# Kernel optimization log

Measured on AMD Instinct MI355X. Metric: run time of the kernel, lower is better.

The kernel has to match this reference:

```python
import jax, jax.numpy as jnp
import numpy as np

# nuScenes-scale config: batch 2, 360x360 BEV grid (1440/4), 128 channels,
# 10 classes, 200 proposals, 3x3 NMS kernel, 40k occupied voxels per sample.
B, H, W_GRID, NUM_CLS, NUM_PROP, NMS_K = 2, 360, 360, 10, 200, 3
C = 128
N_PER_B = 40000
NEG_FILL = -1000000.0  # scatter_nd fill value from to_dense()


def _bev_pos():
    # replicates create_2D_grid: coord = (x_index_along_dim1, y_index_along_dim0)
    xs = jnp.arange(H, dtype=jnp.float32)
    ys = jnp.arange(W_GRID, dtype=jnp.float32)
    by, bx = jnp.meshgrid(xs, ys, indexing='ij')  # by[i,j]=i, bx[i,j]=j
    return jnp.stack([bx, by], axis=-1).reshape(-1, 2)  # [H*W, 2]


def setup_inputs() -> dict:
    key = jax.random.key(0)
    ks = jax.random.split(key, 10)
    # unique spatial locations per batch sample (sparse voxel coords)
    flats = [jax.random.permutation(ks[i], H * W_GRID)[:N_PER_B] for i in range(B)]
    flat = jnp.concatenate(flats)
    b = jnp.repeat(jnp.arange(B), N_PER_B)
    indices = jnp.stack([b, flat // W_GRID, flat % W_GRID], axis=1).astype(jnp.int32)
    features = jax.random.normal(ks[4], (B * N_PER_B, C), jnp.float32)
    # heatmap head (pointwise linears standing in for the submconv stack)
    W_hm1 = jax.random.normal(ks[5], (C, C), jnp.float32) * (2.0 / C) ** 0.5
    b_hm1 = jnp.zeros((C,), jnp.float32)
    W_hm2 = jax.random.normal(ks[6], (C, NUM_CLS), jnp.float32) * (2.0 / C) ** 0.5
    b_hm2 = jnp.full((NUM_CLS,), -2.19, jnp.float32)  # fc[-1].bias.fill_(-2.19)
    # class_encoding: nn.Conv1d(num_class, channels, 1)
    W_cls = jax.random.normal(ks[7], (C, NUM_CLS), jnp.float32) * 0.1
    b_cls = jnp.zeros((C,), jnp.float32)
    return dict(features=features, W_hm1=W_hm1, b_hm1=b_hm1, W_hm2=W_hm2,
                b_hm2=b_hm2, W_cls=W_cls, b_cls=b_cls, indices=indices)


def reference(features, W_hm1, b_hm1, W_hm2, b_hm2, W_cls, b_cls, indices):
    bidx, yi, xi = indices[:, 0], indices[:, 1], indices[:, 2]
    HW = H * W_GRID

    # --- x.dense(): scatter voxel features to dense BEV grid (zero fill) ---
    xd = jnp.zeros((B, H, W_GRID, C), features.dtype).at[bidx, yi, xi].set(features)
    x_flat = xd.reshape(B, HW, C).transpose(0, 2, 1)  # [B, C, HW]

    # --- heatmap head (per-voxel) then to_dense() with -1e6 fill ---
    hm = jax.nn.relu(features @ W_hm1 + b_hm1) @ W_hm2 + b_hm2  # [N, NUM_CLS]
    dense_hm = jnp.full((B, H, W_GRID, NUM_CLS), NEG_FILL, hm.dtype)
    dense_hm = dense_hm.at[bidx, yi, xi].set(hm).transpose(0, 3, 1, 2)  # [B,K,H,W]

    heat = jax.nn.sigmoid(dense_hm)  # detached in original

    # --- NMS-kernel peak extraction ---
    pad = NMS_K // 2
    inner = jax.lax.reduce_window(heat, -jnp.inf, jax.lax.max,
                                  (1, 1, NMS_K, NMS_K), (1, 1, 1, 1), 'VALID')
    local_max = jnp.zeros_like(heat).at[:, :, pad:H - pad, pad:W_GRID - pad].set(inner)
    # pedestrian (8) and traffic_cone (9): kernel size 1
    local_max = local_max.at[:, 8].set(heat[:, 8]).at[:, 9].set(heat[:, 9])
    heat = heat * (heat == local_max)
    heat_f = heat.reshape(B, NUM_CLS, HW)

    # --- top-k proposals over (class, location) ---
    _, top = jax.lax.top_k(heat_f.reshape(B, -1), NUM_PROP)  # [B, P]
    cls = top // HW
    idx = top % HW

    # --- gather proposal features + class encoding ---
    qf = jnp.take_along_axis(x_flat, jnp.broadcast_to(idx[:, None, :], (B, C, NUM_PROP)), axis=2)
    onehot = jax.nn.one_hot(cls, NUM_CLS, dtype=qf.dtype)  # [B, P, K]
    qf = qf + jnp.einsum('ck,bpk->bcp', W_cls, onehot) + b_cls[None, :, None]

    # --- proposal positions and heatmap scores ---
    query_pos = _bev_pos()[idx]  # [B, P, 2]
    qhs = jnp.take_along_axis(heat_f, jnp.broadcast_to(idx[:, None, :], (B, NUM_CLS, NUM_PROP)), axis=2)
    return qf, query_pos, qhs, cls
```

## Files before the change

kernel.cpp:

```cpp
#include <hip/hip_runtime.h>

#define HW 129600
#define WG 360
#define HG 360
#define NCLS 10
#define NPROP 200
#define CDIM 128
#define NROWS 80000
#define NB 2
#define NPB (NROWS / NB)
#define SEL_CAP 4096
#define HBINS 4096
#define RPB 64
#define PSTR 12
#define BPB 32

__device__ __align__(16) const float ZROW[12] = {0.f, 0.f, 0.f, 0.f, 0.f, 0.f,
                                                 0.f, 0.f, 0.f, 0.f, 0.f, 0.f};

__device__ __forceinline__ void lds_cp16(float* l, const float* g) {
  __builtin_amdgcn_global_load_lds(
      (const __attribute__((address_space(1))) void*)g,
      (__attribute__((address_space(3))) void*)l, 16, 0, 0);
}

__device__ __forceinline__ float4 fmax4(float4 a, float4 b) {
  float4 r;
  r.x = fmaxf(a.x, b.x);
  r.y = fmaxf(a.y, b.y);
  r.z = fmaxf(a.z, b.z);
  r.w = fmaxf(a.w, b.w);
  return r;
}

__global__ __launch_bounds__(256, 4) void k_head(
    const float* __restrict__ feat, const float* __restrict__ W1,
    const float* __restrict__ b1, const float* __restrict__ W2,
    const float* __restrict__ b2, const int* __restrict__ idxs,
    float* __restrict__ val_raw, int* __restrict__ rowmap,
    unsigned int* __restrict__ hist, int* __restrict__ sel_cnt) {
  __shared__ __align__(16) float lds_w[3][16 * 128];
  __shared__ __align__(16) float lds_f[3][RPB * 16];
  const int tid = threadIdx.x;
  const int row0 = blockIdx.x * RPB;
  const int tc = tid & 31;
  const int tr = tid >> 5;
  const int wv = tid >> 6;
  const int lane = tid & 63;

  auto stage = [&](int kt, int nb) {
#pragma unroll
    for (int c = 0; c < 2; ++c) {
      const int off = (wv * 2 + c) * 256;
      lds_cp16(&lds_w[nb][off], W1 + kt * 2048 + off + lane * 4);
    }
    {
      const int off = wv * 256;
      const int fidx = off + lane * 4;
      const int r = fidx >> 4, kk = fidx & 15;
      lds_cp16(&lds_f[nb][off],
               feat + (size_t)(row0 + r) * CDIM + kt * 16 + kk);
    }
  };

  stage(0, 0);
  stage(1, 1);
  if (blockIdx.x == 0) {
    uint4* h4 = (uint4*)hist;
    for (int i = tid; i < (NB * HBINS) / 4; i += 256)
      h4[i] = make_uint4(0u, 0u, 0u, 0u);
    if (tid < 2) sel_cnt[tid] = 0;
  }
  if (tid < RPB) {
    int row = row0 + tid;
    int bb = idxs[row * 3 + 0];
    int yy = idxs[row * 3 + 1];
    int xx = idxs[row * 3 + 2];
    rowmap[(size_t)bb * HW + yy * WG + xx] = row;
  }

  float acc[8][4];
#pragma unroll
  for (int r = 0; r < 8; ++r)
#pragma unroll
    for (int c = 0; c < 4; ++c) acc[r][c] = 0.f;

#pragma unroll
  for (int kt = 0; kt < 8; ++kt) {
    const int cb = kt % 3;
    if (kt < 7) {
      asm volatile("s_waitcnt vmcnt(3)" ::: "memory");
    } else {
      asm volatile("s_waitcnt vmcnt(0)" ::: "memory");
    }
    __builtin_amdgcn_sched_barrier(0);
    __builtin_amdgcn_s_barrier();
    __builtin_amdgcn_sched_barrier(0);
    if (kt < 6) stage(kt + 2, (kt + 2) % 3);
#pragma unroll
    for (int kg = 0; kg < 4; ++kg) {
      float4 w0 = *(const float4*)(&lds_w[cb][(kg * 4 + 0) * 128 + tc * 4]);
      float4 w1 = *(const float4*)(&lds_w[cb][(kg * 4 + 1) * 128 + tc * 4]);
      float4 w2 = *(const float4*)(&lds_w[cb][(kg * 4 + 2) * 128 + tc * 4]);
      float4 w3 = *(const float4*)(&lds_w[cb][(kg * 4 + 3) * 128 + tc * 4]);
#pragma unroll
      for (int r = 0; r < 8; ++r) {
        float4 fv = *(const float4*)(&lds_f[cb][(tr * 8 + r) * 16 + kg * 4]);
        acc[r][0] = fmaf(fv.x, w0.x, acc[r][0]);
        acc[r][0] = fmaf(fv.y, w1.x, acc[r][0]);
        acc[r][0] = fmaf(fv.z, w2.x, acc[r][0]);
        acc[r][0] = fmaf(fv.w, w3.x, acc[r][0]);
        acc[r][1] = fmaf(fv.x, w0.y, acc[r][1]);
        acc[r][1] = fmaf(fv.y, w1.y, acc[r][1]);
        acc[r][1] = fmaf(fv.z, w2.y, acc[r][1]);
        acc[r][1] = fmaf(fv.w, w3.y, acc[r][1]);
        acc[r][2] = fmaf(fv.x, w0.z, acc[r][2]);
        acc[r][2] = fmaf(fv.y, w1.z, acc[r][2]);
        acc[r][2] = fmaf(fv.z, w2.z, acc[r][2]);
        acc[r][2] = fmaf(fv.w, w3.z, acc[r][2]);
        acc[r][3] = fmaf(fv.x, w0.w, acc[r][3]);
        acc[r][3] = fmaf(fv.y, w1.w, acc[r][3]);
        acc[r][3] = fmaf(fv.z, w2.w, acc[r][3]);
        acc[r][3] = fmaf(fv.w, w3.w, acc[r][3]);
      }
    }
  }
  __syncthreads();

  float* w2t = &lds_f[0][0];
  for (int i = tid; i < CDIM * NCLS; i += 256) {
    int k = i / NCLS, j = i - k * NCLS;
    w2t[j * 128 + k] = W2[i];
  }
  __syncthreads();

  float* hbuf = &lds_w[0][0];
  float4 b1v = *(const float4*)(b1 + tc * 4);
#pragma unroll
  for (int half = 0; half < 2; ++half) {
    if ((tr >> 2) == half) {
      int ltr = tr & 3;
#pragma unroll
      for (int r = 0; r < 8; ++r) {
        float4 h;
        h.x = fmaxf(acc[r][0] + b1v.x, 0.f);
        h.y = fmaxf(acc[r][1] + b1v.y, 0.f);
        h.z = fmaxf(acc[r][2] + b1v.z, 0.f);
        h.w = fmaxf(acc[r][3] + b1v.w, 0.f);
        *(float4*)(hbuf + (ltr * 8 + r) * 128 + tc * 4) = h;
      }
    }
    __syncthreads();
    for (int o = tid; o < 32 * NCLS; o += 256) {
      int r = o / NCLS, j = o - r * NCLS;
      float s = b2[j];
      for (int i4 = 0; i4 < 32; ++i4) {
        int k4 = (i4 + tid) & 31;
        float4 hv = *(const float4*)(hbuf + r * 128 + k4 * 4);
        float4 wv2 = *(const float4*)(w2t + j * 128 + k4 * 4);
        s = fmaf(hv.x, wv2.x, s);
        s = fmaf(hv.y, wv2.y, s);
        s = fmaf(hv.z, wv2.z, s);
        s = fmaf(hv.w, wv2.w, s);
      }
      float heat = 1.0f / (1.0f + expf(-s));
      int gr = half * 32 + r;
      val_raw[(size_t)(row0 + gr) * PSTR + j] = heat;
    }
    __syncthreads();
  }
}

__global__ __launch_bounds__(256) void k_hist(
    const float* __restrict__ val_raw, const int* __restrict__ idxs,
    const int* __restrict__ rowmap, float* __restrict__ val,
    unsigned int* __restrict__ hist) {
  __shared__ unsigned int lh[HBINS];
  const int tid = threadIdx.x;
  const int row = blockIdx.x * 256 + tid;
  const int blk_b = (blockIdx.x * 256 >= NPB) ? 1 : 0;
  for (int i = tid; i < HBINS; i += 256) lh[i] = 0;
  __syncthreads();

  float v[10];
  int bb = 0;
  const bool valid = row < NROWS;
  if (valid) {
    bb = (row >= NPB) ? 1 : 0;
    const int y = idxs[row * 3 + 1];
    const int x = idxs[row * 3 + 2];
    const int pos = y * WG + x;
    const float* cbase = val_raw + (size_t)row * PSTR;
    float4 c0 = *(const float4*)(cbase + 0);
    float4 c1 = *(const float4*)(cbase + 4);
    float2 c89 = *(const float2*)(cbase + 8);
    const bool interior = (y > 0 && y < HG - 1 && x > 0 && x < WG - 1);
    if (interior) {
      const int dyA[8] = {0, 0, -1, -1, -1, 1, 1, 1};
      const int dxA[8] = {-1, 1, -1, 0, 1, -1, 0, 1};
      float4 m0 = c0, m1 = c1;
      const int* rmb = rowmap + (size_t)bb * HW + pos;
#pragma unroll
      for (int n = 0; n < 8; ++n) {
        const int nrow = rmb[dyA[n] * WG + dxA[n]];
        bool ok =
            ((unsigned)nrow < NROWS) && ((nrow >= NPB) == (bb == 1));
        if (ok) {
          ok = (idxs[nrow * 3 + 1] == y + dyA[n]) &&
               (idxs[nrow * 3 + 2] == x + dxA[n]);
        }
        const float* p = ok ? (val_raw + (size_t)nrow * PSTR) : ZROW;
        m0 = fmax4(m0, *(const float4*)(p + 0));
        m1 = fmax4(m1, *(const float4*)(p + 4));
      }
      v[0] = (c0.x == m0.x) ? c0.x : 0.f;
      v[1] = (c0.y == m0.y) ? c0.y : 0.f;
      v[2] = (c0.z == m0.z) ? c0.z : 0.f;
      v[3] = (c0.w == m0.w) ? c0.w : 0.f;
      v[4] = (c1.x == m1.x) ? c1.x : 0.f;
      v[5] = (c1.y == m1.y) ? c1.y : 0.f;
      v[6] = (c1.z == m1.z) ? c1.z : 0.f;
      v[7] = (c1.w == m1.w) ? c1.w : 0.f;
    } else {
      v[0] = v[1] = v[2] = v[3] = v[4] = v[5] = v[6] = v[7] = 0.f;
    }
    v[8] = c89.x;
    v[9] = c89.y;
    float4 s0 = {v[0], v[1], v[2], v[3]};
    float4 s1 = {v[4], v[5], v[6], v[7]};
    float4 s2 = {v[8], v[9], 0.f, 0.f};
    *(float4*)(val + (size_t)row * PSTR + 0) = s0;
    *(float4*)(val + (size_t)row * PSTR + 4) = s1;
    *(float4*)(val + (size_t)row * PSTR + 8) = s2;
#pragma unroll
    for (int c = 0; c < 10; ++c) {
      if (v[c] > 0.f) {
        unsigned int bin = __float_as_uint(v[c]) >> 18;
        if (bb == blk_b)
          atomicAdd(&lh[bin], 1u);
        else
          atomicAdd(&hist[(size_t)bb * HBINS + bin], 1u);
      }
    }
  }
  __syncthreads();
  unsigned int* gh = hist + (size_t)blk_b * HBINS;
  for (int i = tid; i < HBINS; i += 256) {
    unsigned int c = lh[i];
    if (c) atomicAdd(&gh[i], c);
  }
}

__global__ __launch_bounds__(256) void k_collect(
    const float* __restrict__ val, const int* __restrict__ idxs,
    const unsigned int* __restrict__ hist, unsigned long long* __restrict__ sel,
    int* __restrict__ sel_cnt) {
  __shared__ unsigned int coarse[256];
  __shared__ unsigned int fine16[16];
  __shared__ int sT[2];
  __shared__ int sCi[2];
  const int tid = threadIdx.x;
  for (int bb = 0; bb < NB; ++bb) {
    const unsigned int* h = hist + (size_t)bb * HBINS;
    const uint4* h4 = (const uint4*)(h + tid * 16);
    unsigned int s = 0;
#pragma unroll
    for (int i = 0; i < 4; ++i) {
      uint4 q = h4[i];
      s += q.x + q.y + q.z + q.w;
    }
    if (tid == 0) {
      sCi[bb] = -1;
      sT[bb] = 0;
    }
    coarse[tid] = s;
    __syncthreads();
#pragma unroll
    for (int off = 1; off < 256; off <<= 1) {
      unsigned int vv = (tid + off < 256) ? coarse[tid + off] : 0u;
      __syncthreads();
      coarse[tid] += vv;
      __syncthreads();
    }
    if (coarse[tid] >= NPROP) atomicMax(&sCi[bb], tid);
    __syncthreads();
    const int ci = sCi[bb];
    if (ci >= 0) {
      if (tid < 16) fine16[tid] = h[ci * 16 + tid];
      __syncthreads();
      if (tid == 0) {
        unsigned int cum = (ci + 1 < 256) ? coarse[ci + 1] : 0u;
        int t = 15;
        for (; t > 0; --t) {
          unsigned int c = fine16[t];
          if (cum + c >= NPROP) break;
          cum += c;
        }
        sT[bb] = ci * 16 + t;
      }
    }
    __syncthreads();
  }
  const int row = blockIdx.x * 256 + tid;
  const bool valid = row < NROWS;
  const int bb = (valid && row >= NPB) ? 1 : 0;
  const int T = sT[bb];
  float v[12];
  int pos = 0;
  if (valid) {
    *(float4*)(v + 0) = *(const float4*)(val + (size_t)row * PSTR + 0);
    *(float4*)(v + 4) = *(const float4*)(val + (size_t)row * PSTR + 4);
    *(float4*)(v + 8) = *(const float4*)(val + (size_t)row * PSTR + 8);
    pos = idxs[row * 3 + 1] * WG + idxs[row * 3 + 2];
  }
  const int lane = tid & 63;
#pragma unroll
  for (int cl = 0; cl < 10; ++cl) {
    float vv = valid ? v[cl] : 0.f;
    unsigned int bits = __float_as_uint(vv);
    bool pred = (vv > 0.f) && ((int)(bits >> 18) >= T);
    unsigned long long m0 = __ballot(pred && (bb == 0));
    unsigned long long m1 = __ballot(pred && (bb == 1));
    if (pred) {
      unsigned long long mask = bb ? m1 : m0;
      int leader = __ffsll((unsigned long long)mask) - 1;
      int lb = __popcll(mask & ((1ull << lane) - 1ull));
      int base = 0;
      if (lane == leader) base = atomicAdd(&sel_cnt[bb], (int)__popcll(mask));
      base = __shfl(base, leader, 64);
      unsigned int gidx = (unsigned int)cl * HW + (unsigned int)pos;
      unsigned long long key =
          ((unsigned long long)bits << 32) | (unsigned long long)(~gidx);
      int slot = base + lb;
      if (slot < SEL_CAP) sel[(size_t)bb * SEL_CAP + slot] = key;
    }
  }
}

__global__ __launch_bounds__(256) void k_final(
    const unsigned long long* __restrict__ sel, const int* __restrict__ sel_cnt,
    const float* __restrict__ val, const int* __restrict__ rowmap,
    const float* __restrict__ feat, const float* __restrict__ Wc,
    const float* __restrict__ bc, float* __restrict__ out) {
  __shared__ unsigned long long sk[SEL_CAP];
  __shared__ unsigned long long winners[NPROP];
  __shared__ int wcls[NPROP];
  __shared__ int wrow[NPROP];
  const int b = blockIdx.x / BPB;
  const int part = blockIdx.x % BPB;
  const int tid = threadIdx.x;
  int M = sel_cnt[b];
  if (M > SEL_CAP) M = SEL_CAP;
  for (int i = tid; i < M; i += 256) sk[i] = sel[(size_t)b * SEL_CAP + i];
  __syncthreads();
  for (int i = tid; i < M; i += 256) {
    unsigned long long key = sk[i];
    int rank = 0;
    for (int j = 0; j < M; ++j) rank += (sk[j] > key) ? 1 : 0;
    if (rank < NPROP) winners[rank] = key;
  }
  __syncthreads();
  if (tid < NPROP) {
    unsigned long long key = winners[tid];
    unsigned int gidx = ~((unsigned int)(key & 0xFFFFFFFFull));
    int cls = (int)(gidx / HW);
    int pos = (int)(gidx - (unsigned int)cls * HW);
    wcls[tid] = cls;
    wrow[tid] = rowmap[(size_t)b * HW + pos];
    if (part == 0) {
      int y = pos / WG, x = pos - y * WG;
      out[51200 + ((size_t)b * NPROP + tid) * 2 + 0] = (float)x;
      out[51200 + ((size_t)b * NPROP + tid) * 2 + 1] = (float)y;
      out[56000 + b * NPROP + tid] = (float)cls;
    }
  }
  __syncthreads();
  for (int o = part * 256 + tid; o < NCLS * NPROP; o += BPB * 256) {
    int j = o / NPROP, pp = o - j * NPROP;
    out[52000 + (size_t)b * NCLS * NPROP + o] = val[(size_t)wrow[pp] * PSTR + j];
  }
  for (int o = part * 256 + tid; o < CDIM * NPROP; o += BPB * 256) {
    int c = o / NPROP, pp = o - c * NPROP;
    out[(size_t)b * CDIM * NPROP + o] =
        feat[(size_t)wrow[pp] * CDIM + c] + Wc[c * NCLS + wcls[pp]] + bc[c];
  }
}

extern "C" void kernel_launch(void* const* d_in, const int* in_sizes, int n_in,
                              void* d_out, int out_size, void* d_ws,
                              size_t ws_size, hipStream_t stream) {
  const float* feat = (const float*)d_in[0];
  const float* W1 = (const float*)d_in[1];
  const float* b1 = (const float*)d_in[2];
  const float* W2 = (const float*)d_in[3];
  const float* b2 = (const float*)d_in[4];
  const float* Wc = (const float*)d_in[5];
  const float* bc = (const float*)d_in[6];
  const int* idxs = (const int*)d_in[7];
  float* out = (float*)d_out;

  char* ws = (char*)d_ws;
  unsigned int* hist = (unsigned int*)(ws + 0);
  int* rowmap = (int*)(ws + 32768);
  unsigned long long* sel = (unsigned long long*)(ws + 1069568);
  int* sel_cnt = (int*)(ws + 1135104);
  float* val_raw = (float*)(ws + 1135120);
  float* val = (float*)(ws + 4975120);

  k_head<<<NROWS / RPB, 256, 0, stream>>>(feat, W1, b1, W2, b2, idxs, val_raw,
                                          rowmap, hist, sel_cnt);
  k_hist<<<(NROWS + 255) / 256, 256, 0, stream>>>(val_raw, idxs, rowmap, val,
                                                  hist);
  k_collect<<<(NROWS + 255) / 256, 256, 0, stream>>>(val, idxs, hist, sel,
                                                     sel_cnt);
  k_final<<<NB * BPB, 256, 0, stream>>>(sel, sel_cnt, val, rowmap, feat, Wc, bc,
                                        out);
}
```

Measured before the change: 173.5 us.

## Fuse candidate collection into final top-k kernel with per-block LDS selection

Merges the candidate-collection and final ranking kernels into one. Each final block now computes the histogram threshold for its batch, scans all rows of that batch itself, and appends candidates to shared memory with LDS atomics. This removes one kernel launch, the global selection buffer and its counter, and the global atomics. The cost is that each of the 32 blocks per batch redundantly scans the whole batch. That is a long serial loop per block with little memory parallelism.

```diff
diff --git a/kernel.cpp b/kernel.cpp
--- a/kernel.cpp
+++ b/kernel.cpp
@@ -38,7 +38,7 @@
     const float* __restrict__ b1, const float* __restrict__ W2,
     const float* __restrict__ b2, const int* __restrict__ idxs,
     float* __restrict__ val_raw, int* __restrict__ rowmap,
-    unsigned int* __restrict__ hist, int* __restrict__ sel_cnt) {
+    unsigned int* __restrict__ hist) {
   __shared__ __align__(16) float lds_w[3][16 * 128];
   __shared__ __align__(16) float lds_f[3][RPB * 16];
   const int tid = threadIdx.x;
@@ -69,7 +69,6 @@
     uint4* h4 = (uint4*)hist;
     for (int i = tid; i < (NB * HBINS) / 4; i += 256)
       h4[i] = make_uint4(0u, 0u, 0u, 0u);
-    if (tid < 2) sel_cnt[tid] = 0;
   }
   if (tid < RPB) {
     int row = row0 + tid;
@@ -171,7 +170,7 @@
   }
 }
 
-__global__ __launch_bounds__(256) void k_hist(
+__global__ __launch_bounds__(256) void k_nms(
     const float* __restrict__ val_raw, const int* __restrict__ idxs,
     const int* __restrict__ rowmap, float* __restrict__ val,
     unsigned int* __restrict__ hist) {
@@ -251,17 +250,29 @@
   }
 }
 
-__global__ __launch_bounds__(256) void k_collect(
+__global__ __launch_bounds__(256) void k_sel(
     const float* __restrict__ val, const int* __restrict__ idxs,
-    const unsigned int* __restrict__ hist, unsigned long long* __restrict__ sel,
-    int* __restrict__ sel_cnt) {
+    const unsigned int* __restrict__ hist, const int* __restrict__ rowmap,
+    const float* __restrict__ feat, const float* __restrict__ Wc,
+    const float* __restrict__ bc, float* __restrict__ out) {
+  __shared__ unsigned long long sk[SEL_CAP];
+  __shared__ unsigned long long winners[NPROP];
+  __shared__ int wcls[NPROP];
+  __shared__ int wrow[NPROP];
   __shared__ unsigned int coarse[256];
   __shared__ unsigned int fine16[16];
-  __shared__ int sT[2];
-  __shared__ int sCi[2];
+  __shared__ int sT1, sCi1, lcnt;
+  const int b = blockIdx.x / BPB;
+  const int part = blockIdx.x % BPB;
   const int tid = threadIdx.x;
-  for (int bb = 0; bb < NB; ++bb) {
-    const unsigned int* h = hist + (size_t)bb * HBINS;
+
+  if (tid == 0) {
+    sCi1 = -1;
+    sT1 = 0;
+    lcnt = 0;
+  }
+  {
+    const unsigned int* h = hist + (size_t)b * HBINS;
     const uint4* h4 = (const uint4*)(h + tid * 16);
     unsigned int s = 0;
 #pragma unroll
@@ -269,24 +280,22 @@
       uint4 q = h4[i];
       s += q.x + q.y + q.z + q.w;
     }
-    if (tid == 0) {
-      sCi[bb] = -1;
-      sT[bb] = 0;
-    }
     coarse[tid] = s;
-    __syncthreads();
-#pragma unroll
-    for (int off = 1; off < 256; off <<= 1) {
-      unsigned int vv = (tid + off < 256) ? coarse[tid + off] : 0u;
-      __syncthreads();
-      coarse[tid] += vv;
-      __syncthreads();
-    }
-    if (coarse[tid] >= NPROP) atomicMax(&sCi[bb], tid);
-    __syncthreads();
-    const int ci = sCi[bb];
+  }
+  __syncthreads();
+#pragma unroll
+  for (int off = 1; off < 256; off <<= 1) {
+    unsigned int vv = (tid + off < 256) ? coarse[tid + off] : 0u;
+    __syncthreads();
+    coarse[tid] += vv;
+    __syncthreads();
+  }
+  if (coarse[tid] >= NPROP) atomicMax(&sCi1, tid);
+  __syncthreads();
+  {
+    const int ci = sCi1;
     if (ci >= 0) {
-      if (tid < 16) fine16[tid] = h[ci * 16 + tid];
+      if (tid < 16) fine16[tid] = hist[(size_t)b * HBINS + ci * 16 + tid];
       __syncthreads();
       if (tid == 0) {
         unsigned int cum = (ci + 1 < 256) ? coarse[ci + 1] : 0u;
@@ -296,63 +305,38 @@
           if (cum + c >= NPROP) break;
           cum += c;
         }
-        sT[bb] = ci * 16 + t;
-      }
-    }
-    __syncthreads();
-  }
-  const int row = blockIdx.x * 256 + tid;
-  const bool valid = row < NROWS;
-  const int bb = (valid && row >= NPB) ? 1 : 0;
-  const int T = sT[bb];
-  float v[12];
-  int pos = 0;
-  if (valid) {
-    *(float4*)(v + 0) = *(const float4*)(val + (size_t)row * PSTR + 0);
-    *(float4*)(v + 4) = *(const float4*)(val + (size_t)row * PSTR + 4);
-    *(float4*)(v + 8) = *(const float4*)(val + (size_t)row * PSTR + 8);
-    pos = idxs[row * 3 + 1] * WG + idxs[row * 3 + 2];
-  }
-  const int lane = tid & 63;
-#pragma unroll
-  for (int cl = 0; cl < 10; ++cl) {
-    float vv = valid ? v[cl] : 0.f;
-    unsigned int bits = __float_as_uint(vv);
-    bool pred = (vv > 0.f) && ((int)(bits >> 18) >= T);
-    unsigned long long m0 = __ballot(pred && (bb == 0));
-    unsigned long long m1 = __ballot(pred && (bb == 1));
-    if (pred) {
-      unsigned long long mask = bb ? m1 : m0;
-      int leader = __ffsll((unsigned long long)mask) - 1;
-      int lb = __popcll(mask & ((1ull << lane) - 1ull));
-      int base = 0;
-      if (lane == leader) base = atomicAdd(&sel_cnt[bb], (int)__popcll(mask));
-      base = __shfl(base, leader, 64);
-      unsigned int gidx = (unsigned int)cl * HW + (unsigned int)pos;
-      unsigned long long key =
-          ((unsigned long long)bits << 32) | (unsigned long long)(~gidx);
-      int slot = base + lb;
-      if (slot < SEL_CAP) sel[(size_t)bb * SEL_CAP + slot] = key;
-    }
-  }
-}
-
-__global__ __launch_bounds__(256) void k_final(
-    const unsigned long long* __restrict__ sel, const int* __restrict__ sel_cnt,
-    const float* __restrict__ val, const int* __restrict__ rowmap,
-    const float* __restrict__ feat, const float* __restrict__ Wc,
-    const float* __restrict__ bc, float* __restrict__ out) {
-  __shared__ unsigned long long sk[SEL_CAP];
-  __shared__ unsigned long long winners[NPROP];
-  __shared__ int wcls[NPROP];
-  __shared__ int wrow[NPROP];
-  const int b = blockIdx.x / BPB;
-  const int part = blockIdx.x % BPB;
-  const int tid = threadIdx.x;
-  int M = sel_cnt[b];
+        sT1 = ci * 16 + t;
+      }
+    }
+    __syncthreads();
+  }
+  const int T = sT1;
+
+  for (int r = tid; r < NPB; r += 256) {
+    const int row = b * NPB + r;
+    float4 a0 = *(const float4*)(val + (size_t)row * PSTR + 0);
+    float4 a1 = *(const float4*)(val + (size_t)row * PSTR + 4);
+    float2 a2 = *(const float2*)(val + (size_t)row * PSTR + 8);
+    const float v[10] = {a0.x, a0.y, a0.z, a0.w, a1.x,
+                         a1.y, a1.z, a1.w, a2.x, a2.y};
+    const int pos = idxs[row * 3 + 1] * WG + idxs[row * 3 + 2];
+#pragma unroll
+    for (int cl = 0; cl < 10; ++cl) {
+      unsigned int bits = __float_as_uint(v[cl]);
+      if (v[cl] > 0.f && (int)(bits >> 18) >= T) {
+        int ls = atomicAdd(&lcnt, 1);
+        if (ls < SEL_CAP) {
+          unsigned int gidx = (unsigned int)cl * HW + (unsigned int)pos;
+          sk[ls] =
+              ((unsigned long long)bits << 32) | (unsigned long long)(~gidx);
+        }
+      }
+    }
+  }
+  __syncthreads();
+  int M = lcnt;
   if (M > SEL_CAP) M = SEL_CAP;
-  for (int i = tid; i < M; i += 256) sk[i] = sel[(size_t)b * SEL_CAP + i];
-  __syncthreads();
+
   for (int i = tid; i < M; i += 256) {
     unsigned long long key = sk[i];
     int rank = 0;
@@ -402,17 +386,13 @@
   char* ws = (char*)d_ws;
   unsigned int* hist = (unsigned int*)(ws + 0);
   int* rowmap = (int*)(ws + 32768);
-  unsigned long long* sel = (unsigned long long*)(ws + 1069568);
-  int* sel_cnt = (int*)(ws + 1135104);
-  float* val_raw = (float*)(ws + 1135120);
-  float* val = (float*)(ws + 4975120);
+  float* val_raw = (float*)(ws + 1069568);
+  float* val = (float*)(ws + 4909568);
 
   k_head<<<NROWS / RPB, 256, 0, stream>>>(feat, W1, b1, W2, b2, idxs, val_raw,
-                                          rowmap, hist, sel_cnt);
-  k_hist<<<(NROWS + 255) / 256, 256, 0, stream>>>(val_raw, idxs, rowmap, val,
-                                                  hist);
-  k_collect<<<(NROWS + 255) / 256, 256, 0, stream>>>(val, idxs, hist, sel,
-                                                     sel_cnt);
-  k_final<<<NB * BPB, 256, 0, stream>>>(sel, sel_cnt, val, rowmap, feat, Wc, bc,
-                                        out);
-}
+                                          rowmap, hist);
+  k_nms<<<(NROWS + 255) / 256, 256, 0, stream>>>(val_raw, idxs, rowmap, val,
+                                                 hist);
+  k_sel<<<NB * BPB, 256, 0, stream>>>(val, idxs, hist, rowmap, feat, Wc, bc,
+                                      out);
+}
```

New measurement: 263.0 us. +51.6%, slower.

## Enlarge head GEMM tile to 128 rows with 8x8 per-thread register blocking

Applied to the files above, without the earlier changes.

The first-layer GEMM tile in k_head doubles from 64 to 128 rows per block, and each thread now computes an 8x8 output micro-tile instead of 8x4. The staging, wait counts and the second-layer epilogue (now four quarters) are adjusted to match. This raises arithmetic intensity per LDS load and halves the block count, which cuts the per-block overhead of W1 staging. In exchange it uses more registers and LDS, lowers occupancy (launch bounds drop from 4 to 3) and leaves fewer blocks to spread across CUs.

```diff
diff --git a/kernel.cpp b/kernel.cpp
--- a/kernel.cpp
+++ b/kernel.cpp
@@ -11,7 +11,7 @@
 #define NPB (NROWS / NB)
 #define SEL_CAP 4096
 #define HBINS 4096
-#define RPB 64
+#define RPB 128
 #define PSTR 12
 #define BPB 32
 
@@ -33,7 +33,7 @@
   return r;
 }
 
-__global__ __launch_bounds__(256, 4) void k_head(
+__global__ __launch_bounds__(256, 3) void k_head(
     const float* __restrict__ feat, const float* __restrict__ W1,
     const float* __restrict__ b1, const float* __restrict__ W2,
     const float* __restrict__ b2, const int* __restrict__ idxs,
@@ -43,8 +43,8 @@
   __shared__ __align__(16) float lds_f[3][RPB * 16];
   const int tid = threadIdx.x;
   const int row0 = blockIdx.x * RPB;
-  const int tc = tid & 31;
-  const int tr = tid >> 5;
+  const int tc = tid & 15;
+  const int tr = tid >> 4;
   const int wv = tid >> 6;
   const int lane = tid & 63;
 
@@ -54,8 +54,9 @@
       const int off = (wv * 2 + c) * 256;
       lds_cp16(&lds_w[nb][off], W1 + kt * 2048 + off + lane * 4);
     }
-    {
-      const int off = wv * 256;
+#pragma unroll
+    for (int c = 0; c < 2; ++c) {
+      const int off = (wv * 2 + c) * 256;
       const int fidx = off + lane * 4;
       const int r = fidx >> 4, kk = fidx & 15;
       lds_cp16(&lds_f[nb][off],
@@ -79,17 +80,17 @@
     rowmap[(size_t)bb * HW + yy * WG + xx] = row;
   }
 
-  float acc[8][4];
+  float acc[8][8];
 #pragma unroll
   for (int r = 0; r < 8; ++r)
 #pragma unroll
-    for (int c = 0; c < 4; ++c) acc[r][c] = 0.f;
+    for (int c = 0; c < 8; ++c) acc[r][c] = 0.f;
 
 #pragma unroll
   for (int kt = 0; kt < 8; ++kt) {
     const int cb = kt % 3;
     if (kt < 7) {
-      asm volatile("s_waitcnt vmcnt(3)" ::: "memory");
+      asm volatile("s_waitcnt vmcnt(4)" ::: "memory");
     } else {
       asm volatile("s_waitcnt vmcnt(0)" ::: "memory");
     }
@@ -99,29 +100,49 @@
     if (kt < 6) stage(kt + 2, (kt + 2) % 3);
 #pragma unroll
     for (int kg = 0; kg < 4; ++kg) {
-      float4 w0 = *(const float4*)(&lds_w[cb][(kg * 4 + 0) * 128 + tc * 4]);
-      float4 w1 = *(const float4*)(&lds_w[cb][(kg * 4 + 1) * 128 + tc * 4]);
-      float4 w2 = *(const float4*)(&lds_w[cb][(kg * 4 + 2) * 128 + tc * 4]);
-      float4 w3 = *(const float4*)(&lds_w[cb][(kg * 4 + 3) * 128 + tc * 4]);
+      float4 a0 = *(const float4*)(&lds_w[cb][(kg * 4 + 0) * 128 + tc * 8]);
+      float4 a1 = *(const float4*)(&lds_w[cb][(kg * 4 + 1) * 128 + tc * 8]);
+      float4 a2 = *(const float4*)(&lds_w[cb][(kg * 4 + 2) * 128 + tc * 8]);
+      float4 a3 = *(const float4*)(&lds_w[cb][(kg * 4 + 3) * 128 + tc * 8]);
+      float4 b0 = *(const float4*)(&lds_w[cb][(kg * 4 + 0) * 128 + tc * 8 + 4]);
+      float4 b1q = *(const float4*)(&lds_w[cb][(kg * 4 + 1) * 128 + tc * 8 + 4]);
+      float4 b2q = *(const float4*)(&lds_w[cb][(kg * 4 + 2) * 128 + tc * 8 + 4]);
+      float4 b3q = *(const float4*)(&lds_w[cb][(kg * 4 + 3) * 128 + tc * 8 + 4]);
 #pragma unroll
       for (int r = 0; r < 8; ++r) {
         float4 fv = *(const float4*)(&lds_f[cb][(tr * 8 + r) * 16 + kg * 4]);
-        acc[r][0] = fmaf(fv.x, w0.x, acc[r][0]);
-        acc[r][0] = fmaf(fv.y, w1.x, acc[r][0]);
-        acc[r][0] = fmaf(fv.z, w2.x, acc[r][0]);
-        acc[r][0] = fmaf(fv.w, w3.x, acc[r][0]);
-        acc[r][1] = fmaf(fv.x, w0.y, acc[r][1]);
-        acc[r][1] = fmaf(fv.y, w1.y, acc[r][1]);
-        acc[r][1] = fmaf(fv.z, w2.y, acc[r][1]);
-        acc[r][1] = fmaf(fv.w, w3.y, acc[r][1]);
-        acc[r][2] = fmaf(fv.x, w0.z, acc[r][2]);
-        acc[r][2] = fmaf(fv.y, w1.z, acc[r][2]);
-        acc[r][2] = fmaf(fv.z, w2.z, acc[r][2]);
-        acc[r][2] = fmaf(fv.w, w3.z, acc[r][2]);
-        acc[r][3] = fmaf(fv.x, w0.w, acc[r][3]);
-        acc[r][3] = fmaf(fv.y, w1.w, acc[r][3]);
-        acc[r][3] = fmaf(fv.z, w2.w, acc[r][3]);
-        acc[r][3] = fmaf(fv.w, w3.w, acc[r][3]);
+        acc[r][0] = fmaf(fv.x, a0.x, acc[r][0]);
+        acc[r][0] = fmaf(fv.y, a1.x, acc[r][0]);
+        acc[r][0] = fmaf(fv.z, a2.x, acc[r][0]);
+        acc[r][0] = fmaf(fv.w, a3.x, acc[r][0]);
+        acc[r][1] = fmaf(fv.x, a0.y, acc[r][1]);
+        acc[r][1] = fmaf(fv.y, a1.y, acc[r][1]);
+        acc[r][1] = fmaf(fv.z, a2.y, acc[r][1]);
+        acc[r][1] = fmaf(fv.w, a3.y, acc[r][1]);
+        acc[r][2] = fmaf(fv.x, a0.z, acc[r][2]);
+        acc[r][2] = fmaf(fv.y, a1.z, acc[r][2]);
+        acc[r][2] = fmaf(fv.z, a2.z, acc[r][2]);
+        acc[r][2] = fmaf(fv.w, a3.z, acc[r][2]);
+        acc[r][3] = fmaf(fv.x, a0.w, acc[r][3]);
+        acc[r][3] = fmaf(fv.y, a1.w, acc[r][3]);
+        acc[r][3] = fmaf(fv.z, a2.w, acc[r][3]);
+        acc[r][3] = fmaf(fv.w, a3.w, acc[r][3]);
+        acc[r][4] = fmaf(fv.x, b0.x, acc[r][4]);
+        acc[r][4] = fmaf(fv.y, b1q.x, acc[r][4]);
+        acc[r][4] = fmaf(fv.z, b2q.x, acc[r][4]);
+        acc[r][4] = fmaf(fv.w, b3q.x, acc[r][4]);
+        acc[r][5] = fmaf(fv.x, b0.y, acc[r][5]);
+        acc[r][5] = fmaf(fv.y, b1q.y, acc[r][5]);
+        acc[r][5] = fmaf(fv.z, b2q.y, acc[r][5]);
+        acc[r][5] = fmaf(fv.w, b3q.y, acc[r][5]);
+        acc[r][6] = fmaf(fv.x, b0.z, acc[r][6]);
+        acc[r][6] = fmaf(fv.y, b1q.z, acc[r][6]);
+        acc[r][6] = fmaf(fv.z, b2q.z, acc[r][6]);
+        acc[r][6] = fmaf(fv.w, b3q.z, acc[r][6]);
+        acc[r][7] = fmaf(fv.x, b0.w, acc[r][7]);
+        acc[r][7] = fmaf(fv.y, b1q.w, acc[r][7]);
+        acc[r][7] = fmaf(fv.z, b2q.w, acc[r][7]);
+        acc[r][7] = fmaf(fv.w, b3q.w, acc[r][7]);
       }
     }
   }
@@ -135,19 +156,26 @@
   __syncthreads();
 
   float* hbuf = &lds_w[0][0];
-  float4 b1v = *(const float4*)(b1 + tc * 4);
-#pragma unroll
-  for (int half = 0; half < 2; ++half) {
-    if ((tr >> 2) == half) {
+  float4 b1a = *(const float4*)(b1 + tc * 8);
+  float4 b1b = *(const float4*)(b1 + tc * 8 + 4);
+#pragma unroll
+  for (int q = 0; q < 4; ++q) {
+    if ((tr >> 2) == q) {
       int ltr = tr & 3;
 #pragma unroll
       for (int r = 0; r < 8; ++r) {
         float4 h;
-        h.x = fmaxf(acc[r][0] + b1v.x, 0.f);
-        h.y = fmaxf(acc[r][1] + b1v.y, 0.f);
-        h.z = fmaxf(acc[r][2] + b1v.z, 0.f);
-        h.w = fmaxf(acc[r][3] + b1v.w, 0.f);
-        *(float4*)(hbuf + (ltr * 8 + r) * 128 + tc * 4) = h;
+        h.x = fmaxf(acc[r][0] + b1a.x, 0.f);
+        h.y = fmaxf(acc[r][1] + b1a.y, 0.f);
+        h.z = fmaxf(acc[r][2] + b1a.z, 0.f);
+        h.w = fmaxf(acc[r][3] + b1a.w, 0.f);
+        *(float4*)(hbuf + (ltr * 8 + r) * 128 + tc * 8) = h;
+        float4 h2;
+        h2.x = fmaxf(acc[r][4] + b1b.x, 0.f);
+        h2.y = fmaxf(acc[r][5] + b1b.y, 0.f);
+        h2.z = fmaxf(acc[r][6] + b1b.z, 0.f);
+        h2.w = fmaxf(acc[r][7] + b1b.w, 0.f);
+        *(float4*)(hbuf + (ltr * 8 + r) * 128 + tc * 8 + 4) = h2;
       }
     }
     __syncthreads();
@@ -164,7 +192,7 @@
         s = fmaf(hv.w, wv2.w, s);
       }
       float heat = 1.0f / (1.0f + expf(-s));
-      int gr = half * 32 + r;
+      int gr = q * 32 + r;
       val_raw[(size_t)(row0 + gr) * PSTR + j] = heat;
     }
     __syncthreads();
```

New measurement: 180.1 us. 1.04x slower.
